# Optimization experiments

Measured on AMD Instinct MI355X. Metric: run time of the kernel, lower is better.

## Reference

```python
import jax, jax.numpy as jnp
import numpy as np

K = 3          # kernel_size
STRIDE = 1
PAD = 1
NUM_BASIS = 8
DEGREE = 3
M = NUM_BASIS + DEGREE   # number of basis slots (11)
EPS = 1e-5               # BatchNorm2d default eps


def _unfold(x):
    # x: [B,C,H,W] -> patches [B,C,L,K*K] (L = Ho*Wo spatial positions, last dim = kernel pos)
    x = jnp.pad(x, ((0, 0), (0, 0), (PAD, PAD), (PAD, PAD)))
    B, C, H, W = x.shape
    Ho = (H - K) // STRIDE + 1
    Wo = (W - K) // STRIDE + 1
    ii = (jnp.arange(Ho) * STRIDE)[:, None] + jnp.arange(K)[None, :]   # [Ho,K]
    jj = (jnp.arange(Wo) * STRIDE)[:, None] + jnp.arange(K)[None, :]   # [Wo,K]
    p = x[:, :, ii[:, None, :, None], jj[None, :, None, :]]           # [B,C,Ho,Wo,K,K]
    return p.reshape(B, C, Ho * Wo, K * K), Ho, Wo


def _bspline_basis(u):
    # Vectorized Cox-de Boor recursion, faithful to the module's in-place update
    # (entries j >= M-d keep their stale lower-degree values, as in the original).
    # u: [...,] in (0,1) -> basis [..., M]
    knots = jnp.linspace(0.0, 1.0, M + 1).astype(u.dtype)              # 12 knots
    b = ((u[..., None] >= knots[:M]) & (u[..., None] < knots[1:M + 1])).astype(u.dtype)
    for d in range(1, DEGREE + 1):
        n = M - d
        j = np.arange(n)
        den1 = knots[j + d] - knots[j]
        den2 = knots[j + d + 1] - knots[j + 1]
        alpha = jnp.where(den1 != 0, (u[..., None] - knots[j]) / jnp.where(den1 != 0, den1, 1.0), 0.0)
        beta = jnp.where(den2 != 0, (knots[j + d + 1] - u[..., None]) / jnp.where(den2 != 0, den2, 1.0), 0.0)
        upd = alpha * b[..., :n] + beta * b[..., 1:n + 1]
        b = jnp.concatenate([upd, b[..., n:]], axis=-1)
    return b


def setup_inputs() -> dict:
    key = jax.random.key(0)
    k1, k2, k3 = jax.random.split(key, 3)
    B, C_in, C_out, H, W = 8, 64, 128, 56, 56
    x = jax.random.normal(k1, (B, C_in, H, W), dtype=jnp.float32)
    # Xavier-uniform-like scale for control points [O, C, K*K, M]
    fan = C_in * K * K * M + C_out
    bound_cp = float(np.sqrt(6.0 / fan))
    control_points = jax.random.uniform(k2, (C_out, C_in, K * K, M), minval=-bound_cp, maxval=bound_cp, dtype=jnp.float32)
    bound_w = float(np.sqrt(6.0 / (C_in * K * K + C_out * K * K)))
    conv_w = jax.random.uniform(k3, (C_out, C_in, K, K), minval=-bound_w, maxval=bound_w, dtype=jnp.float32)
    conv_b = jnp.zeros((C_out,), dtype=jnp.float32)
    bn_gamma = jnp.ones((C_out,), dtype=jnp.float32)
    bn_beta = jnp.zeros((C_out,), dtype=jnp.float32)
    return {"x": x, "control_points": control_points, "conv_w": conv_w,
            "conv_b": conv_b, "bn_gamma": bn_gamma, "bn_beta": bn_beta}


def reference(x, control_points, conv_w, conv_b, bn_gamma, bn_beta):
    patches, Ho, Wo = _unfold(x)                 # [B,C,L,K2]
    u = jax.nn.sigmoid(patches)
    basis = _bspline_basis(u)                    # [B,C,L,K2,M]
    # spline output: contract in_channels, kernel positions, basis index
    spline = jnp.einsum('bclkn,ockn->bol', basis, control_points)
    B = x.shape[0]
    O = control_points.shape[0]
    spline = spline.reshape(B, O, Ho, Wo)
    conv = jax.lax.conv_general_dilated(x, conv_w, (STRIDE, STRIDE), [(PAD, PAD), (PAD, PAD)],
                                        dimension_numbers=('NCHW', 'OIHW', 'NCHW'))
    out = spline + conv + conv_b[None, :, None, None]
    # Dropout2d is identity in eval mode. BatchNorm2d with batch statistics (training default).
    mean = out.mean(axis=(0, 2, 3), keepdims=True)
    var = out.var(axis=(0, 2, 3), keepdims=True)
    out = (out - mean) * jax.lax.rsqrt(var + EPS)
    return out * bn_gamma[None, :, None, None] + bn_beta[None, :, None, None]
```

## Files before the change

### kernel.cpp

```cpp
#include <hip/hip_runtime.h>
#include <math.h>

#define CIN   64
#define COUT  128
#define HW    56
#define L_    3136
#define KTOT  6912
#define TH    8
#define TW    8
#define HALO_W 10
#define NPIX  100
#define CSTR  (NPIX*16 + 32)
#define G8_SIZE (8*CSTR)
#define G4_SIZE (4*CSTR)
#define BUF_SIZE (G8_SIZE+G4_SIZE)

#define BP_BYTES (COUT * KTOT * 2)
#define PART_OFF BP_BYTES
#define SS_OFF   (PART_OFF + 2048 * 4)

typedef __attribute__((ext_vector_type(8))) short bf16x8;
typedef __attribute__((ext_vector_type(4))) float f32x4;
typedef unsigned long long u64;

#define BLOAD(dst, addr) \
    asm volatile("global_load_dwordx4 %0, %1, off" : "=v"(dst) : "v"(addr))
#define XLOAD(dst, addr) \
    asm volatile("global_load_dword %0, %1, off" : "=v"(dst) : "v"(addr))

__device__ __forceinline__ unsigned short f2bf(float f) {
    unsigned int u = __float_as_uint(f);
    return (unsigned short)((u + 0x7FFFu + ((u >> 16) & 1u)) >> 16);
}
__device__ __forceinline__ unsigned int pk2(float a, float b) {
    return (unsigned int)f2bf(a) | ((unsigned int)f2bf(b) << 16);
}

__device__ __forceinline__ void eval_store(float xv, char* g8rec, char* g4half) {
    float u  = 1.0f / (1.0f + __expf(-xv));
    float tt = u * 11.0f;
    int s = (int)floorf(tt);
    s = (s > 10) ? 10 : s;
    float xf  = tt - (float)s;
    float x2  = xf * xf, x3 = x2 * xf;
    float omx = 1.0f - xf;
    const float i6 = 1.0f / 6.0f;
    float w3 = x3 * i6;
    float w2 = fmaf(fmaf(fmaf(-3.0f, xf, 3.0f), xf, 3.0f), xf, 1.0f) * i6;
    float w1 = fmaf(fmaf(3.0f, xf, -6.0f), x2, 4.0f) * i6;
    float w0 = omx * omx * omx * i6;

    unsigned int b0 = f2bf(w0), b1 = f2bf(w1), b2 = f2bf(w2), b3 = f2bf(w3);
    unsigned int slot[8];
#pragma unroll
    for (int j = 0; j < 8; j++) {
        unsigned int v = 0;
        v = (s == j)     ? b3 : v;
        v = (s == j + 1) ? b2 : v;
        v = (s == j + 2) ? b1 : v;
        v = (s == j + 3) ? b0 : v;
        slot[j] = v;
    }
    uint4 rec;
    rec.x = slot[0] | (slot[1] << 16);
    rec.y = slot[2] | (slot[3] << 16);
    rec.z = slot[4] | (slot[5] << 16);
    rec.w = slot[6] | (slot[7] << 16);
    *reinterpret_cast<uint4*>(g8rec) = rec;

    float y = tt - 8.0f;
    float f8 = 0.0f;
    f8 = (s == 8)  ? 0.5f * y * y : f8;
    f8 = (s == 9)  ? 0.5f * fmaf(-2.0f * y, y, fmaf(6.0f, y, -3.0f)) : f8;
    f8 = (s == 10) ? 0.5f * (3.0f - y) * (3.0f - y) : f8;
    float z = tt - 9.0f;
    float f9 = 0.0f;
    f9 = (s == 9)  ? z : f9;
    f9 = (s == 10) ? 2.0f - z : f9;
    float f10 = (s == 10) ? 1.0f : 0.0f;
    *reinterpret_cast<uint2*>(g4half) = make_uint2(pk2(f8, f9), pk2(f10, xv));
}

__global__ __launch_bounds__(256) void k_packB(const float* __restrict__ cp,
                                               const float* __restrict__ w,
                                               unsigned short* __restrict__ Bp) {
    int idx = blockIdx.x * 256 + threadIdx.x;
    if (idx >= COUT * KTOT) return;
    int kstep = idx >> 12;
    int rem   = idx & 4095;
    int o     = rem >> 5;
    int e32   = rem & 31;
    int ch = kstep / 27, sc = kstep - ch * 27;
    int ktap = sc / 3, ph = sc - ktap * 3;
    int c, n;
    if (ph < 2) { c = ch * 8 + ph * 4 + (e32 >> 3); n = e32 & 7; }
    else        { int sub = e32 & 7; c = ch * 8 + (e32 >> 3) * 2 + (sub >> 2); n = 8 + (sub & 3); }
    float v;
    if (n < 11) v = cp[(((size_t)o * CIN + c) * 9 + ktap) * 11 + n];
    else        v = w[((size_t)o * CIN + c) * 9 + ktap];
    Bp[idx] = f2bf(v);
}

__global__ __launch_bounds__(256, 2) void k_main(const float* __restrict__ x,
                                                 const unsigned short* __restrict__ Bp,
                                                 float* __restrict__ out) {
    __shared__ char lds[2 * BUF_SIZE];

    const int bid  = blockIdx.x;
    const int b    = bid / 49;
    const int tile = bid - b * 49;
    const int th   = tile / 7;
    const int tw   = tile - th * 7;
    const int t    = threadIdx.x;
    const int lane = t & 63;
    const int wid  = t >> 6;

    const bool valid = (t < 200);
    const int p     = (t < 100) ? t : (t - 100);
    const int hi100 = (t >= 100) ? 1 : 0;
    const int ph_  = p / 10, pw_ = p - ph_ * 10;
    const int hg = th * TH - 1 + ph_;
    const int wg = tw * TW - 1 + pw_;
    const bool inb = valid && (hg >= 0) && (hg < HW) && (wg >= 0) && (wg < HW);
    const u64 xadv = inb ? (u64)8 * L_ * 4 : 0;
    u64 px[4];
#pragma unroll
    for (int r = 0; r < 4; r++) {
        int c0 = 2 * r + hi100;
        px[r] = inb ? ((u64)x + (((u64)b * CIN + c0) * L_ + (u64)hg * HW + wg) * 4)
                    : (u64)x;
    }

    const int q   = lane >> 4;
    const int r15 = lane & 15;
    int P[4];
#pragma unroll
    for (int mi = 0; mi < 4; mi++) {
        int lh = mi * 2 + (r15 >> 3);
        int lw = r15 & 7;
        P[mi] = (lh * HALO_W + lw) * 16 + q * CSTR;
    }
    const int obase = wid * 32 + r15;

    const u64 bend = (u64)Bp + BP_BYTES;
    u64 pa0 = (u64)Bp + ((u64)obase * 64) + ((u64)q * 16);
    u64 pa1 = pa0 + 1024;

    f32x4 acc[4][2];
#pragma unroll
    for (int mi = 0; mi < 4; mi++)
#pragma unroll
        for (int ni = 0; ni < 2; ni++) acc[mi][ni] = (f32x4){0.f, 0.f, 0.f, 0.f};

    float xa[4];
    XLOAD(xa[0], px[0]); XLOAD(xa[1], px[1]);
    XLOAD(xa[2], px[2]); XLOAD(xa[3], px[3]);
#pragma unroll
    for (int r = 0; r < 4; r++) px[r] += xadv;
    asm volatile("s_waitcnt vmcnt(0)");
    __builtin_amdgcn_sched_barrier(0);
    if (valid) {
#pragma unroll
        for (int r = 0; r < 4; r++) {
            float va = inb ? xa[r] : 0.0f;
            int c = 2 * r + hi100;
            eval_store(va, &lds[c * CSTR + p * 16],
                       &lds[G8_SIZE + r * CSTR + p * 16 + hi100 * 8]);
        }
    }
    __syncthreads();

    bf16x8 breg0[9], breg1[9];
#pragma unroll
    for (int s = 0; s < 9; s++) {
        BLOAD(breg0[s], pa0);
        BLOAD(breg1[s], pa1);
        pa0 += 8192; pa1 += 8192;
    }

#pragma unroll 1
    for (int ch = 0; ch < 8; ch++) {
        XLOAD(xa[0], px[0]); XLOAD(xa[1], px[1]);
        XLOAD(xa[2], px[2]); XLOAD(xa[3], px[3]);
        if (ch < 6) {
#pragma unroll
            for (int r = 0; r < 4; r++) px[r] += xadv;
        }

        char* abuf = &lds[(ch & 1) * BUF_SIZE];
        char* nbuf = &lds[((ch + 1) & 1) * BUF_SIZE];

        bf16x8 areg[3][4];
        auto aread = [&](int s, bf16x8 (&a)[4]) {
            int k = s / 3, bp = s - k * 3;
            int ki = k / 3, kj = k - ki * 3;
            int poff = (ki * HALO_W + kj) * 16;
            int aoff = (bp == 2) ? (G8_SIZE + poff) : (bp * 4 * CSTR + poff);
#pragma unroll
            for (int mi = 0; mi < 4; mi++)
                a[mi] = *reinterpret_cast<const bf16x8*>(abuf + P[mi] + aoff);
        };
        aread(0, areg[0]);
        aread(1, areg[1]);

#pragma unroll
        for (int s = 0; s < 27; s++) {
            if (s + 2 < 27) aread(s + 2, areg[(s + 2) % 3]);
            asm volatile("s_waitcnt vmcnt(16)");
            __builtin_amdgcn_sched_barrier(0);
            const int bs = s % 9;
#pragma unroll
            for (int mi = 0; mi < 4; mi++) {
                acc[mi][0] = __builtin_amdgcn_mfma_f32_16x16x32_bf16(areg[s % 3][mi], breg0[bs], acc[mi][0], 0, 0, 0);
                acc[mi][1] = __builtin_amdgcn_mfma_f32_16x16x32_bf16(areg[s % 3][mi], breg1[bs], acc[mi][1], 0, 0, 0);
            }
            BLOAD(breg0[bs], pa0);
            BLOAD(breg1[bs], pa1);
            pa0 += 8192; if (pa0 >= bend) pa0 -= BP_BYTES;
            pa1 += 8192; if (pa1 >= bend) pa1 -= BP_BYTES;
        }

        if (ch < 7 && valid) {
#pragma unroll
            for (int r = 0; r < 4; r++) {
                float va = inb ? xa[r] : 0.0f;
                int c = 2 * r + hi100;
                eval_store(va, &nbuf[c * CSTR + p * 16],
                           &nbuf[G8_SIZE + r * CSTR + p * 16 + hi100 * 8]);
            }
        }
        __syncthreads();
    }

#pragma unroll
    for (int ni = 0; ni < 2; ni++) {
        int o = obase + ni * 16;
#pragma unroll
        for (int mi = 0; mi < 4; mi++) {
            int lh = mi * 2 + (q >> 1);
            int lw0 = (q & 1) * 4;
            int lg = (th * TH + lh) * HW + tw * TW + lw0;
            float4 v;
            v.x = acc[mi][ni][0];
            v.y = acc[mi][ni][1];
            v.z = acc[mi][ni][2];
            v.w = acc[mi][ni][3];
            *reinterpret_cast<float4*>(&out[(size_t)(b * COUT + o) * L_ + lg]) = v;
        }
    }
}

__global__ __launch_bounds__(256) void k_part(const float* __restrict__ s,
                                              float* __restrict__ part) {
    const int slab = blockIdx.x;
    const float4* p4 = reinterpret_cast<const float4*>(s + (size_t)slab * L_);
    const int t = threadIdx.x;
    float sum = 0.f, sq = 0.f;
    for (int i = t; i < L_ / 4; i += 256) {
        float4 v = p4[i];
        sum += v.x + v.y + v.z + v.w;
        sq  += v.x * v.x + v.y * v.y + v.z * v.z + v.w * v.w;
    }
    __shared__ float rs[256], rq[256];
    rs[t] = sum; rq[t] = sq;
    __syncthreads();
    for (int off = 128; off > 0; off >>= 1) {
        if (t < off) { rs[t] += rs[t + off]; rq[t] += rq[t + off]; }
        __syncthreads();
    }
    if (t == 0) { part[slab] = rs[0]; part[1024 + slab] = rq[0]; }
}

__global__ __launch_bounds__(128) void k_final(const float* __restrict__ part,
                                               const float* __restrict__ gamma,
                                               const float* __restrict__ beta,
                                               float* __restrict__ ss) {
    int o = threadIdx.x;
    float sum = 0.f, sq = 0.f;
#pragma unroll
    for (int b = 0; b < 8; b++) {
        sum += part[b * COUT + o];
        sq  += part[1024 + b * COUT + o];
    }
    float n = (float)(8 * L_);
    float mean = sum / n;
    float var  = sq / n - mean * mean;
    float scale = gamma[o] * rsqrtf(var + 1e-5f);
    ss[o]        = scale;
    ss[COUT + o] = beta[o] - mean * scale;
}

__global__ __launch_bounds__(256) void k_norm(float* __restrict__ out,
                                              const float* __restrict__ ss) {
    const int n4 = 8 * COUT * L_ / 4;
    for (int i = blockIdx.x * 256 + threadIdx.x; i < n4; i += gridDim.x * 256) {
        int o = ((i * 4) / L_) & (COUT - 1);
        float sc = ss[o], sh = ss[COUT + o];
        float4 v = reinterpret_cast<float4*>(out)[i];
        v.x = fmaf(v.x, sc, sh);
        v.y = fmaf(v.y, sc, sh);
        v.z = fmaf(v.z, sc, sh);
        v.w = fmaf(v.w, sc, sh);
        reinterpret_cast<float4*>(out)[i] = v;
    }
}

extern "C" void kernel_launch(void* const* d_in, const int* in_sizes, int n_in,
                              void* d_out, int out_size, void* d_ws, size_t ws_size,
                              hipStream_t stream) {
    const float* x     = (const float*)d_in[0];
    const float* cp    = (const float*)d_in[1];
    const float* w     = (const float*)d_in[2];
    const float* gamma = (const float*)d_in[4];
    const float* beta  = (const float*)d_in[5];
    float* out = (float*)d_out;

    unsigned short* Bp = (unsigned short*)d_ws;
    float* part = (float*)((char*)d_ws + PART_OFF);
    float* ss   = (float*)((char*)d_ws + SS_OFF);

    k_packB<<<(COUT * KTOT + 255) / 256, 256, 0, stream>>>(cp, w, Bp);
    k_main<<<8 * 49, 256, 0, stream>>>(x, Bp, out);
    k_part<<<1024, 256, 0, stream>>>(out, part);
    k_final<<<1, 128, 0, stream>>>(part, gamma, beta, ss);
    k_norm<<<2048, 256, 0, stream>>>(out, ss);
}
```

Measured before the change: 86.13 us.

## Split the K reduction across two blocks per tile, summing partials in later passes

Splits the input-channel reduction of the main GEMM across two blocks per tile. Each block writes its partial output into either the output buffer or a workspace buffer, which doubles the grid from 392 to 784 blocks and gives better CU occupancy on the large GPU. The statistics and normalization passes then read and add both partial buffers, which adds extra memory traffic. It also drops the LDS row padding and shortens the A-register prefetch depth from 2 to 1. The split path is enabled only when the workspace is large enough.

New measurement: 89.09 us. 1.03x slower.

```diff
diff --git a/kernel.cpp b/kernel.cpp
--- a/kernel.cpp
+++ b/kernel.cpp
@@ -10,14 +10,19 @@
 #define TW    8
 #define HALO_W 10
 #define NPIX  100
-#define CSTR  (NPIX*16 + 32)
+#define CSTR  (NPIX*16)
 #define G8_SIZE (8*CSTR)
 #define G4_SIZE (4*CSTR)
 #define BUF_SIZE (G8_SIZE+G4_SIZE)
 
-#define BP_BYTES (COUT * KTOT * 2)
-#define PART_OFF BP_BYTES
-#define SS_OFF   (PART_OFF + 2048 * 4)
+#define BP_BYTES  (COUT * KTOT * 2)
+#define OUT_BYTES (8 * COUT * L_ * 4)
+#define P1_OFF    BP_BYTES
+#define PARTS_OFF (P1_OFF + OUT_BYTES)
+#define SSS_OFF   (PARTS_OFF + 2048 * 4)
+#define WS_NEEDED (SSS_OFF + 1024 * 4)
+#define PARTF_OFF BP_BYTES
+#define SSF_OFF   (PARTF_OFF + 2048 * 4)
 
 typedef __attribute__((ext_vector_type(8))) short bf16x8;
 typedef __attribute__((ext_vector_type(4))) float f32x4;
@@ -103,12 +108,19 @@
 
 __global__ __launch_bounds__(256, 2) void k_main(const float* __restrict__ x,
                                                  const unsigned short* __restrict__ Bp,
-                                                 float* __restrict__ out) {
+                                                 float* __restrict__ dst0,
+                                                 float* __restrict__ dst1,
+                                                 int ksplit) {
     __shared__ char lds[2 * BUF_SIZE];
 
     const int bid  = blockIdx.x;
-    const int b    = bid / 49;
-    const int tile = bid - b * 49;
+    const int kh   = ksplit ? (bid & 1) : 0;
+    const int tb   = ksplit ? (bid >> 1) : bid;
+    const int nch  = ksplit ? 4 : 8;
+    float* dst     = kh ? dst1 : dst0;
+
+    const int b    = tb / 49;
+    const int tile = tb - b * 49;
     const int th   = tile / 7;
     const int tw   = tile - th * 7;
     const int t    = threadIdx.x;
@@ -126,7 +138,7 @@
     u64 px[4];
 #pragma unroll
     for (int r = 0; r < 4; r++) {
-        int c0 = 2 * r + hi100;
+        int c0 = kh * 32 + 2 * r + hi100;
         px[r] = inb ? ((u64)x + (((u64)b * CIN + c0) * L_ + (u64)hg * HW + wg) * 4)
                     : (u64)x;
     }
@@ -143,7 +155,7 @@
     const int obase = wid * 32 + r15;
 
     const u64 bend = (u64)Bp + BP_BYTES;
-    u64 pa0 = (u64)Bp + ((u64)obase * 64) + ((u64)q * 16);
+    u64 pa0 = (u64)Bp + (u64)kh * 108 * 8192 + ((u64)obase * 64) + ((u64)q * 16);
     u64 pa1 = pa0 + 1024;
 
     f32x4 acc[4][2];
@@ -179,18 +191,18 @@
     }
 
 #pragma unroll 1
-    for (int ch = 0; ch < 8; ch++) {
+    for (int cr = 0; cr < nch; cr++) {
         XLOAD(xa[0], px[0]); XLOAD(xa[1], px[1]);
         XLOAD(xa[2], px[2]); XLOAD(xa[3], px[3]);
-        if (ch < 6) {
+        if (cr < nch - 2) {
 #pragma unroll
             for (int r = 0; r < 4; r++) px[r] += xadv;
         }
 
-        char* abuf = &lds[(ch & 1) * BUF_SIZE];
-        char* nbuf = &lds[((ch + 1) & 1) * BUF_SIZE];
-
-        bf16x8 areg[3][4];
+        char* abuf = &lds[(cr & 1) * BUF_SIZE];
+        char* nbuf = &lds[((cr + 1) & 1) * BUF_SIZE];
+
+        bf16x8 areg[2][4];
         auto aread = [&](int s, bf16x8 (&a)[4]) {
             int k = s / 3, bp = s - k * 3;
             int ki = k / 3, kj = k - ki * 3;
@@ -201,18 +213,17 @@
                 a[mi] = *reinterpret_cast<const bf16x8*>(abuf + P[mi] + aoff);
         };
         aread(0, areg[0]);
-        aread(1, areg[1]);
 
 #pragma unroll
         for (int s = 0; s < 27; s++) {
-            if (s + 2 < 27) aread(s + 2, areg[(s + 2) % 3]);
+            if (s + 1 < 27) aread(s + 1, areg[(s + 1) & 1]);
             asm volatile("s_waitcnt vmcnt(16)");
             __builtin_amdgcn_sched_barrier(0);
             const int bs = s % 9;
 #pragma unroll
             for (int mi = 0; mi < 4; mi++) {
-                acc[mi][0] = __builtin_amdgcn_mfma_f32_16x16x32_bf16(areg[s % 3][mi], breg0[bs], acc[mi][0], 0, 0, 0);
-                acc[mi][1] = __builtin_amdgcn_mfma_f32_16x16x32_bf16(areg[s % 3][mi], breg1[bs], acc[mi][1], 0, 0, 0);
+                acc[mi][0] = __builtin_amdgcn_mfma_f32_16x16x32_bf16(areg[s & 1][mi], breg0[bs], acc[mi][0], 0, 0, 0);
+                acc[mi][1] = __builtin_amdgcn_mfma_f32_16x16x32_bf16(areg[s & 1][mi], breg1[bs], acc[mi][1], 0, 0, 0);
             }
             BLOAD(breg0[bs], pa0);
             BLOAD(breg1[bs], pa1);
@@ -220,7 +231,7 @@
             pa1 += 8192; if (pa1 >= bend) pa1 -= BP_BYTES;
         }
 
-        if (ch < 7 && valid) {
+        if (cr < nch - 1 && valid) {
 #pragma unroll
             for (int r = 0; r < 4; r++) {
                 float va = inb ? xa[r] : 0.0f;
@@ -231,6 +242,9 @@
         }
         __syncthreads();
     }
+
+    asm volatile("s_waitcnt vmcnt(0)");
+    __builtin_amdgcn_sched_barrier(0);
 
 #pragma unroll
     for (int ni = 0; ni < 2; ni++) {
@@ -245,21 +259,33 @@
             v.y = acc[mi][ni][1];
             v.z = acc[mi][ni][2];
             v.w = acc[mi][ni][3];
-            *reinterpret_cast<float4*>(&out[(size_t)(b * COUT + o) * L_ + lg]) = v;
-        }
-    }
-}
-
-__global__ __launch_bounds__(256) void k_part(const float* __restrict__ s,
-                                              float* __restrict__ part) {
+            *reinterpret_cast<float4*>(&dst[(size_t)(b * COUT + o) * L_ + lg]) = v;
+        }
+    }
+}
+
+__global__ __launch_bounds__(256) void k_part(const float* __restrict__ s0,
+                                              const float* __restrict__ s1,
+                                              float* __restrict__ part,
+                                              int split) {
     const int slab = blockIdx.x;
-    const float4* p4 = reinterpret_cast<const float4*>(s + (size_t)slab * L_);
+    const float4* p0 = reinterpret_cast<const float4*>(s0 + (size_t)slab * L_);
+    const float4* p1 = reinterpret_cast<const float4*>(s1 + (size_t)slab * L_);
     const int t = threadIdx.x;
     float sum = 0.f, sq = 0.f;
-    for (int i = t; i < L_ / 4; i += 256) {
-        float4 v = p4[i];
-        sum += v.x + v.y + v.z + v.w;
-        sq  += v.x * v.x + v.y * v.y + v.z * v.z + v.w * v.w;
+    if (split) {
+        for (int i = t; i < L_ / 4; i += 256) {
+            float4 a = p0[i], c = p1[i];
+            float vx = a.x + c.x, vy = a.y + c.y, vz = a.z + c.z, vw = a.w + c.w;
+            sum += vx + vy + vz + vw;
+            sq  += vx * vx + vy * vy + vz * vz + vw * vw;
+        }
+    } else {
+        for (int i = t; i < L_ / 4; i += 256) {
+            float4 a = p0[i];
+            sum += a.x + a.y + a.z + a.w;
+            sq  += a.x * a.x + a.y * a.y + a.z * a.z + a.w * a.w;
+        }
     }
     __shared__ float rs[256], rq[256];
     rs[t] = sum; rq[t] = sq;
@@ -291,12 +317,18 @@
 }
 
 __global__ __launch_bounds__(256) void k_norm(float* __restrict__ out,
-                                              const float* __restrict__ ss) {
+                                              const float* __restrict__ p1,
+                                              const float* __restrict__ ss,
+                                              int split) {
     const int n4 = 8 * COUT * L_ / 4;
     for (int i = blockIdx.x * 256 + threadIdx.x; i < n4; i += gridDim.x * 256) {
         int o = ((i * 4) / L_) & (COUT - 1);
         float sc = ss[o], sh = ss[COUT + o];
-        float4 v = reinterpret_cast<float4*>(out)[i];
+        float4 v = reinterpret_cast<const float4*>(out)[i];
+        if (split) {
+            float4 w = reinterpret_cast<const float4*>(p1)[i];
+            v.x += w.x; v.y += w.y; v.z += w.z; v.w += w.w;
+        }
         v.x = fmaf(v.x, sc, sh);
         v.y = fmaf(v.y, sc, sh);
         v.z = fmaf(v.z, sc, sh);
@@ -315,13 +347,16 @@
     const float* beta  = (const float*)d_in[5];
     float* out = (float*)d_out;
 
+    const int split = (ws_size >= (size_t)WS_NEEDED) ? 1 : 0;
+
     unsigned short* Bp = (unsigned short*)d_ws;
-    float* part = (float*)((char*)d_ws + PART_OFF);
-    float* ss   = (float*)((char*)d_ws + SS_OFF);
+    float* p1   = (float*)((char*)d_ws + P1_OFF);
+    float* part = (float*)((char*)d_ws + (split ? PARTS_OFF : PARTF_OFF));
+    float* ss   = (float*)((char*)d_ws + (split ? SSS_OFF : SSF_OFF));
 
     k_packB<<<(COUT * KTOT + 255) / 256, 256, 0, stream>>>(cp, w, Bp);
-    k_main<<<8 * 49, 256, 0, stream>>>(x, Bp, out);
-    k_part<<<1024, 256, 0, stream>>>(out, part);
+    k_main<<<split ? 784 : 392, 256, 0, stream>>>(x, Bp, out, p1, split);
+    k_part<<<1024, 256, 0, stream>>>(out, p1, part, split);
     k_final<<<1, 128, 0, stream>>>(part, gamma, beta, ss);
-    k_norm<<<2048, 256, 0, stream>>>(out, ss);
-}
+    k_norm<<<2048, 256, 0, stream>>>(out, p1, ss, split);
+}
```

## Fuse BatchNorm partial statistics into main conv kernel via atomics

Applied to the files above, without the earlier changes.

Removes the separate k_part reduction kernel. The main kernel now accumulates per-channel sum and sum-of-squares from its register accumulators, reduces them across lanes with shuffles, and atomically adds them into a zeroed partial buffer. This avoids re-reading the whole output tensor and one kernel launch. It adds a memset, float atomics with nondeterministic summation order, a remapped block-to-batch order, and drops the min-blocks-per-CU launch bound.

Measured after the change: 83.19 us. 1.04x faster.

```diff
diff --git a/kernel.cpp b/kernel.cpp
--- a/kernel.cpp
+++ b/kernel.cpp
@@ -101,14 +101,15 @@
     Bp[idx] = f2bf(v);
 }
 
-__global__ __launch_bounds__(256, 2) void k_main(const float* __restrict__ x,
-                                                 const unsigned short* __restrict__ Bp,
-                                                 float* __restrict__ out) {
+__global__ __launch_bounds__(256) void k_main(const float* __restrict__ x,
+                                              const unsigned short* __restrict__ Bp,
+                                              float* __restrict__ out,
+                                              float* __restrict__ part) {
     __shared__ char lds[2 * BUF_SIZE];
 
     const int bid  = blockIdx.x;
-    const int b    = bid / 49;
-    const int tile = bid - b * 49;
+    const int b    = bid & 7;
+    const int tile = bid >> 3;
     const int th   = tile / 7;
     const int tw   = tile - th * 7;
     const int t    = threadIdx.x;
@@ -232,6 +233,7 @@
         __syncthreads();
     }
 
+    float psum[2] = {0.f, 0.f}, psq[2] = {0.f, 0.f};
 #pragma unroll
     for (int ni = 0; ni < 2; ni++) {
         int o = obase + ni * 16;
@@ -246,29 +248,25 @@
             v.z = acc[mi][ni][2];
             v.w = acc[mi][ni][3];
             *reinterpret_cast<float4*>(&out[(size_t)(b * COUT + o) * L_ + lg]) = v;
-        }
-    }
-}
-
-__global__ __launch_bounds__(256) void k_part(const float* __restrict__ s,
-                                              float* __restrict__ part) {
-    const int slab = blockIdx.x;
-    const float4* p4 = reinterpret_cast<const float4*>(s + (size_t)slab * L_);
-    const int t = threadIdx.x;
-    float sum = 0.f, sq = 0.f;
-    for (int i = t; i < L_ / 4; i += 256) {
-        float4 v = p4[i];
-        sum += v.x + v.y + v.z + v.w;
-        sq  += v.x * v.x + v.y * v.y + v.z * v.z + v.w * v.w;
-    }
-    __shared__ float rs[256], rq[256];
-    rs[t] = sum; rq[t] = sq;
-    __syncthreads();
-    for (int off = 128; off > 0; off >>= 1) {
-        if (t < off) { rs[t] += rs[t + off]; rq[t] += rq[t + off]; }
-        __syncthreads();
-    }
-    if (t == 0) { part[slab] = rs[0]; part[1024 + slab] = rq[0]; }
+            psum[ni] += v.x + v.y + v.z + v.w;
+            psq[ni]  += v.x * v.x + v.y * v.y + v.z * v.z + v.w * v.w;
+        }
+    }
+#pragma unroll
+    for (int ni = 0; ni < 2; ni++) {
+        psum[ni] += __shfl_xor(psum[ni], 16);
+        psum[ni] += __shfl_xor(psum[ni], 32);
+        psq[ni]  += __shfl_xor(psq[ni], 16);
+        psq[ni]  += __shfl_xor(psq[ni], 32);
+    }
+    if (q == 0) {
+#pragma unroll
+        for (int ni = 0; ni < 2; ni++) {
+            int o = obase + ni * 16;
+            atomicAdd(&part[b * COUT + o], psum[ni]);
+            atomicAdd(&part[1024 + b * COUT + o], psq[ni]);
+        }
+    }
 }
 
 __global__ __launch_bounds__(128) void k_final(const float* __restrict__ part,
@@ -319,9 +317,9 @@
     float* part = (float*)((char*)d_ws + PART_OFF);
     float* ss   = (float*)((char*)d_ws + SS_OFF);
 
+    hipMemsetAsync(part, 0, 2048 * sizeof(float), stream);
     k_packB<<<(COUT * KTOT + 255) / 256, 256, 0, stream>>>(cp, w, Bp);
-    k_main<<<8 * 49, 256, 0, stream>>>(x, Bp, out);
-    k_part<<<1024, 256, 0, stream>>>(out, part);
+    k_main<<<8 * 49, 256, 0, stream>>>(x, Bp, out, part);
     k_final<<<1, 128, 0, stream>>>(part, gamma, beta, ss);
     k_norm<<<2048, 256, 0, stream>>>(out, ss);
 }
```
